# Kernel tuning notes

Measured on AMD Instinct MI355X. Metric: run time of the kernel, lower is better.

## Reference

```python
import jax, jax.numpy as jnp
import numpy as np

N = 4096          # nodes
IN_F = 256        # in_features (divisible by 4)
OUT_F = 64        # out_features per head
HEADS = 4
ALPHA = 0.2       # LeakyReLU negative slope
NEG_INF = -9e15   # same masking constant as the torch code


def make_quaternion_mul(kernel):
    """kernel: [IN_F//4, OUT_F] -> hamilton: [IN_F, OUT_F].
    Mirrors the torch make_quaternion_mul (split along dim=1 into r,i,j,k)."""
    r, i, j, k = jnp.split(kernel, 4, axis=1)
    r2 = jnp.concatenate([r, -i, -j, -k], axis=1)
    i2 = jnp.concatenate([i,  r, -k,  j], axis=1)
    j2 = jnp.concatenate([j,  k,  r, -i], axis=1)
    k2 = jnp.concatenate([k, -j,  i,  r], axis=1)
    return jnp.concatenate([r2, i2, j2, k2], axis=0)


def setup_inputs() -> dict:
    key = jax.random.key(0)
    k1, k2, k3, k4 = jax.random.split(key, 4)
    x = jax.random.normal(k1, (N, IN_F), dtype=jnp.float32)
    # Glorot-ish init for quaternion kernels: [H, IN_F//4, OUT_F]
    stdv = np.sqrt(6.0 / (IN_F // 4 + OUT_F)).astype(np.float32)
    W_heads = jax.random.uniform(k2, (HEADS, IN_F // 4, OUT_F), dtype=jnp.float32,
                                 minval=-stdv, maxval=stdv)
    a_heads = jax.random.normal(k3, (HEADS, 2 * OUT_F), dtype=jnp.float32) * 0.1
    adj = (jax.random.uniform(k4, (N, N)) < 0.005).astype(jnp.float32)
    adj = jnp.maximum(adj, jnp.eye(N, dtype=jnp.float32))
    return {"x": x, "adj": adj, "W_heads": W_heads, "a_heads": a_heads}


def reference(x, adj, W_heads, a_heads):
    mask = adj > 0  # [N, N]

    def head(Wk, ak):
        hamilton = make_quaternion_mul(Wk)                # [IN_F, OUT_F]
        h = x @ hamilton                                  # [N, OUT_F]
        # e[i,j] = leakyrelu(h_i . a[:F] + h_j . a[F:]) -- equivalent to the
        # repeat/concat construction without materializing [N*N, 2F].
        e_src = h @ ak[:OUT_F]                            # [N]
        e_dst = h @ ak[OUT_F:]                            # [N]
        e = jax.nn.leaky_relu(e_src[:, None] + e_dst[None, :], negative_slope=ALPHA)
        att = jax.nn.softmax(jnp.where(mask, e, NEG_INF), axis=1)  # [N, N]
        return att @ h                                    # [N, OUT_F]

    outs = jax.vmap(head)(W_heads, a_heads)               # [H, N, OUT_F]
    out = jnp.transpose(outs, (1, 0, 2)).reshape(N, HEADS * OUT_F)
    return jax.nn.elu(out)  # concat=True path
```

## Files before the change

### kernel.cpp

```cpp
#include <hip/hip_runtime.h>

#define N 4096
#define IN_F 256
#define OUT_F 64
#define HEADS 4
#define ALPHA 0.2f
#define SEG 64
#define LSTRIDE 320

typedef __attribute__((ext_vector_type(8))) short short8;
typedef __attribute__((ext_vector_type(4))) float f32x4;

__device__ __forceinline__ unsigned short f2bf(float f) {
    unsigned u = __builtin_bit_cast(unsigned, f);
    u += 0x7fffu + ((u >> 16) & 1u);
    return (unsigned short)(u >> 16);
}

__device__ __forceinline__ float bf2f(unsigned short u) {
    return __builtin_bit_cast(float, (unsigned)u << 16);
}

__global__ __launch_bounds__(256) void k_main(const float* __restrict__ x,
                                              const float* __restrict__ adj,
                                              const float* __restrict__ W,
                                              const float* __restrict__ a,
                                              unsigned short* __restrict__ hb,
                                              float* __restrict__ esp,
                                              float* __restrict__ edp,
                                              int* __restrict__ lists) {
    __shared__ int s_seg[4][SEG];
    __shared__ int s_cnt[4];
    __shared__ int s_all[4 * SEG];

    const int wave = threadIdx.x >> 6, lane = threadIdx.x & 63;
    const int i = blockIdx.x;

    if (wave == (i & 3)) {
        const int gw = i;
        const int rg = gw >> 4;
        const int hd = (gw >> 2) & 3;
        const int cq = gw & 3;
        const int m0 = rg * 16;
        const int r16 = lane & 15, g = lane >> 4;

        const int   comp_t[4][4] = {{0,1,2,3},{1,0,3,2},{2,3,0,1},{3,2,1,0}};
        const float sign_t[4][4] = {{1.f,-1.f,-1.f,-1.f},
                                    {1.f, 1.f,-1.f, 1.f},
                                    {1.f, 1.f, 1.f,-1.f},
                                    {1.f,-1.f, 1.f, 1.f}};

        const float* xrow = x + (size_t)(m0 + r16) * IN_F + g * 8;
        short8 af[8];
#pragma unroll
        for (int kk = 0; kk < 8; ++kk) {
            const float4 u0 = *reinterpret_cast<const float4*>(xrow + kk * 32);
            const float4 u1 = *reinterpret_cast<const float4*>(xrow + kk * 32 + 4);
            short8 t;
            t[0] = (short)f2bf(u0.x); t[1] = (short)f2bf(u0.y);
            t[2] = (short)f2bf(u0.z); t[3] = (short)f2bf(u0.w);
            t[4] = (short)f2bf(u1.x); t[5] = (short)f2bf(u1.y);
            t[6] = (short)f2bf(u1.z); t[7] = (short)f2bf(u1.w);
            af[kk] = t;
        }

        short8 bfr[8];
#pragma unroll
        for (int kk = 0; kk < 8; ++kk) {
            const int q = kk >> 1;
            const int kr0 = (kk & 1) * 32 + g * 8;
            const float s = sign_t[q][cq];
            const int c = comp_t[q][cq];
            const float* wp = W + (size_t)(hd * 64 + kr0) * 64 + c * 16 + r16;
            short8 t;
#pragma unroll
            for (int j = 0; j < 8; ++j) t[j] = (short)f2bf(s * wp[j * 64]);
            bfr[kk] = t;
        }

        f32x4 acc = (f32x4){0.f, 0.f, 0.f, 0.f};
#pragma unroll
        for (int kk = 0; kk < 8; ++kk)
            acc = __builtin_amdgcn_mfma_f32_16x16x32_bf16(af[kk], bfr[kk], acc, 0, 0, 0);

        const int f = cq * 16 + r16;
        const float as = a[hd * 128 + f];
        const float ad = a[hd * 128 + 64 + f];
        float p[4], q2[4];
#pragma unroll
        for (int j = 0; j < 4; ++j) {
            const float v = acc[j];
            hb[(size_t)(m0 + g * 4 + j) * (HEADS * OUT_F) + hd * 64 + f] = f2bf(v);
            p[j] = v * as;
            q2[j] = v * ad;
        }
#pragma unroll
        for (int off = 1; off < 16; off <<= 1) {
#pragma unroll
            for (int j = 0; j < 4; ++j) {
                p[j] += __shfl_xor(p[j], off);
                q2[j] += __shfl_xor(q2[j], off);
            }
        }
        if (r16 == 0) {
#pragma unroll
            for (int j = 0; j < 4; ++j) {
                const int row = m0 + g * 4 + j;
                esp[row * 16 + hd * 4 + cq] = p[j];
                edp[row * 16 + hd * 4 + cq] = q2[j];
            }
        }
    }

    const uint4* arow = reinterpret_cast<const uint4*>(adj + (size_t)i * N) + wave * 256;
    uint4 av[4];
#pragma unroll
    for (int c = 0; c < 4; ++c) av[c] = arow[c * 64 + lane];

    const unsigned long long lmask_lt = (lane == 63) ? ~0ull >> 1
                                                     : (1ull << lane) - 1ull;
    int base = 0;
#pragma unroll
    for (int c = 0; c < 4; ++c) {
#pragma unroll
        for (int s = 0; s < 4; ++s) {
            const unsigned v = (s == 0) ? av[c].x : (s == 1) ? av[c].y
                             : (s == 2) ? av[c].z : av[c].w;
            const bool hit = v != 0u;
            const unsigned long long mk = __ballot(hit);
            if (hit) {
                const int pos = base + __popcll(mk & lmask_lt);
                if (pos < SEG)
                    s_seg[wave][pos] = wave * 1024 + c * 256 + lane * 4 + s;
            }
            base += __popcll(mk);
        }
    }
    if (lane == 0) s_cnt[wave] = base < SEG ? base : SEG;
    __syncthreads();

    const int c0 = s_cnt[0], c1 = s_cnt[1], c2 = s_cnt[2], c3 = s_cnt[3];
    const int wbase = (wave > 0 ? c0 : 0) + (wave > 1 ? c1 : 0) + (wave > 2 ? c2 : 0);
    const int wcnt = s_cnt[wave];
    if (lane < wcnt) s_all[wbase + lane] = s_seg[wave][lane];
    __syncthreads();
    const int cnt = c0 + c1 + c2 + c3;

    if (threadIdx.x == 0) lists[(size_t)i * LSTRIDE] = cnt;
    for (int t = threadIdx.x; t < cnt; t += 256)
        lists[(size_t)i * LSTRIDE + 1 + t] = s_all[t];
}

__global__ __launch_bounds__(256) void k_out(const unsigned short* __restrict__ hb,
                                             const float* __restrict__ esp,
                                             const float* __restrict__ edp,
                                             const int* __restrict__ lists,
                                             float* __restrict__ out) {
    __shared__ int   s_all[4 * SEG];
    __shared__ float s_z[4][4 * SEG];

    const int wave = threadIdx.x >> 6;
    const int lane = threadIdx.x & 63;
    const int i = blockIdx.x;

    const int cnt = lists[(size_t)i * LSTRIDE];
    for (int t = threadIdx.x; t < cnt; t += 256)
        s_all[t] = lists[(size_t)i * LSTRIDE + 1 + t];
    __syncthreads();

    const int hd = wave;
    const float4 es4 = *reinterpret_cast<const float4*>(&esp[i * 16 + hd * 4]);
    const float es = (es4.x + es4.y) + (es4.z + es4.w);
    float mh = -3.0e38f;
    for (int e = lane; e < cnt; e += 64) {
        const int j = s_all[e];
        const float4 ed4 = *reinterpret_cast<const float4*>(&edp[j * 16 + hd * 4]);
        const float ed = (ed4.x + ed4.y) + (ed4.z + ed4.w);
        float z = es + ed;
        z = z > 0.f ? z : ALPHA * z;
        s_z[hd][e] = z;
        mh = fmaxf(mh, z);
    }
#pragma unroll
    for (int off = 32; off > 0; off >>= 1) mh = fmaxf(mh, __shfl_xor(mh, off));

    float lsum = 0.f, acc = 0.f;
    int e = 0;
    for (; e + 4 <= cnt; e += 4) {
        const int j0 = s_all[e], j1 = s_all[e + 1], j2 = s_all[e + 2], j3 = s_all[e + 3];
        const unsigned short u0 = hb[(size_t)j0 * 256 + threadIdx.x];
        const unsigned short u1 = hb[(size_t)j1 * 256 + threadIdx.x];
        const unsigned short u2 = hb[(size_t)j2 * 256 + threadIdx.x];
        const unsigned short u3 = hb[(size_t)j3 * 256 + threadIdx.x];
        const float w0 = __expf(s_z[hd][e]     - mh);
        const float w1 = __expf(s_z[hd][e + 1] - mh);
        const float w2 = __expf(s_z[hd][e + 2] - mh);
        const float w3 = __expf(s_z[hd][e + 3] - mh);
        lsum += w0 + w1 + w2 + w3;
        acc = fmaf(w0, bf2f(u0), acc);
        acc = fmaf(w1, bf2f(u1), acc);
        acc = fmaf(w2, bf2f(u2), acc);
        acc = fmaf(w3, bf2f(u3), acc);
    }
    for (; e < cnt; ++e) {
        const int j = s_all[e];
        const unsigned short u = hb[(size_t)j * 256 + threadIdx.x];
        const float w = __expf(s_z[hd][e] - mh);
        lsum += w;
        acc = fmaf(w, bf2f(u), acc);
    }

    const float v = acc / lsum;
    out[(size_t)i * 256 + threadIdx.x] = v > 0.f ? v : __expf(v) - 1.f;
}

extern "C" void kernel_launch(void* const* d_in, const int* in_sizes, int n_in,
                              void* d_out, int out_size, void* d_ws, size_t ws_size,
                              hipStream_t stream) {
    const float* x   = (const float*)d_in[0];
    const float* adj = (const float*)d_in[1];
    const float* W   = (const float*)d_in[2];
    const float* a   = (const float*)d_in[3];
    float* out = (float*)d_out;

    float* ws  = (float*)d_ws;
    float* esp = ws;
    float* edp = esp + N * 16;
    unsigned short* hb = (unsigned short*)(edp + N * 16);
    int* lists = (int*)(hb + (size_t)N * 256);

    k_main<<<N, 256, 0, stream>>>(x, adj, W, a, hb, esp, edp, lists);
    k_out<<<N, 256, 0, stream>>>(hb, esp, edp, lists, out);
}
```

Before: 38.07 us.

## Process four rows per block in both kernels and use all waves for GEMM

Both kernels now launch N/4 blocks, each looping over four adjacency rows, instead of one block per row. In k_main every wave of a block now does one GEMM tile, where before only one wave per block did. The aim is to cut block launch and scheduling overhead and idle waves. In exchange there are fewer blocks, so less parallelism and latency hiding across CUs, and each block runs its row loop serially with extra barriers.

```diff
diff --git a/kernel.cpp b/kernel.cpp
--- a/kernel.cpp
+++ b/kernel.cpp
@@ -7,6 +7,7 @@
 #define ALPHA 0.2f
 #define SEG 64
 #define LSTRIDE 320
+#define RPB 4
 
 typedef __attribute__((ext_vector_type(8))) short short8;
 typedef __attribute__((ext_vector_type(4))) float f32x4;
@@ -34,15 +35,15 @@
     __shared__ int s_all[4 * SEG];
 
     const int wave = threadIdx.x >> 6, lane = threadIdx.x & 63;
-    const int i = blockIdx.x;
-
-    if (wave == (i & 3)) {
-        const int gw = i;
+    const int g = blockIdx.x;
+
+    {
+        const int gw = g * 4 + wave;
         const int rg = gw >> 4;
         const int hd = (gw >> 2) & 3;
         const int cq = gw & 3;
         const int m0 = rg * 16;
-        const int r16 = lane & 15, g = lane >> 4;
+        const int r16 = lane & 15, g4 = lane >> 4;
 
         const int   comp_t[4][4] = {{0,1,2,3},{1,0,3,2},{2,3,0,1},{3,2,1,0}};
         const float sign_t[4][4] = {{1.f,-1.f,-1.f,-1.f},
@@ -50,7 +51,7 @@
                                     {1.f, 1.f, 1.f,-1.f},
                                     {1.f,-1.f, 1.f, 1.f}};
 
-        const float* xrow = x + (size_t)(m0 + r16) * IN_F + g * 8;
+        const float* xrow = x + (size_t)(m0 + r16) * IN_F + g4 * 8;
         short8 af[8];
 #pragma unroll
         for (int kk = 0; kk < 8; ++kk) {
@@ -68,7 +69,7 @@
 #pragma unroll
         for (int kk = 0; kk < 8; ++kk) {
             const int q = kk >> 1;
-            const int kr0 = (kk & 1) * 32 + g * 8;
+            const int kr0 = (kk & 1) * 32 + g4 * 8;
             const float s = sign_t[q][cq];
             const int c = comp_t[q][cq];
             const float* wp = W + (size_t)(hd * 64 + kr0) * 64 + c * 16 + r16;
@@ -90,7 +91,7 @@
 #pragma unroll
         for (int j = 0; j < 4; ++j) {
             const float v = acc[j];
-            hb[(size_t)(m0 + g * 4 + j) * (HEADS * OUT_F) + hd * 64 + f] = f2bf(v);
+            hb[(size_t)(m0 + g4 * 4 + j) * (HEADS * OUT_F) + hd * 64 + f] = f2bf(v);
             p[j] = v * as;
             q2[j] = v * ad;
         }
@@ -105,50 +106,55 @@
         if (r16 == 0) {
 #pragma unroll
             for (int j = 0; j < 4; ++j) {
-                const int row = m0 + g * 4 + j;
+                const int row = m0 + g4 * 4 + j;
                 esp[row * 16 + hd * 4 + cq] = p[j];
                 edp[row * 16 + hd * 4 + cq] = q2[j];
             }
         }
     }
 
-    const uint4* arow = reinterpret_cast<const uint4*>(adj + (size_t)i * N) + wave * 256;
-    uint4 av[4];
-#pragma unroll
-    for (int c = 0; c < 4; ++c) av[c] = arow[c * 64 + lane];
-
     const unsigned long long lmask_lt = (lane == 63) ? ~0ull >> 1
                                                      : (1ull << lane) - 1ull;
-    int base = 0;
-#pragma unroll
-    for (int c = 0; c < 4; ++c) {
-#pragma unroll
-        for (int s = 0; s < 4; ++s) {
-            const unsigned v = (s == 0) ? av[c].x : (s == 1) ? av[c].y
-                             : (s == 2) ? av[c].z : av[c].w;
-            const bool hit = v != 0u;
-            const unsigned long long mk = __ballot(hit);
-            if (hit) {
-                const int pos = base + __popcll(mk & lmask_lt);
-                if (pos < SEG)
-                    s_seg[wave][pos] = wave * 1024 + c * 256 + lane * 4 + s;
+    for (int r = 0; r < RPB; ++r) {
+        const int i = g * RPB + r;
+        if (r) __syncthreads();
+
+        const uint4* arow = reinterpret_cast<const uint4*>(adj + (size_t)i * N) + wave * 256;
+        uint4 av[4];
+#pragma unroll
+        for (int c = 0; c < 4; ++c) av[c] = arow[c * 64 + lane];
+
+        int base = 0;
+#pragma unroll
+        for (int c = 0; c < 4; ++c) {
+#pragma unroll
+            for (int s = 0; s < 4; ++s) {
+                const unsigned v = (s == 0) ? av[c].x : (s == 1) ? av[c].y
+                                 : (s == 2) ? av[c].z : av[c].w;
+                const bool hit = v != 0u;
+                const unsigned long long mk = __ballot(hit);
+                if (hit) {
+                    const int pos = base + __popcll(mk & lmask_lt);
+                    if (pos < SEG)
+                        s_seg[wave][pos] = wave * 1024 + c * 256 + lane * 4 + s;
+                }
+                base += __popcll(mk);
             }
-            base += __popcll(mk);
-        }
+        }
+        if (lane == 0) s_cnt[wave] = base < SEG ? base : SEG;
+        __syncthreads();
+
+        const int c0 = s_cnt[0], c1 = s_cnt[1], c2 = s_cnt[2], c3 = s_cnt[3];
+        const int wbase = (wave > 0 ? c0 : 0) + (wave > 1 ? c1 : 0) + (wave > 2 ? c2 : 0);
+        const int wcnt = s_cnt[wave];
+        if (lane < wcnt) s_all[wbase + lane] = s_seg[wave][lane];
+        __syncthreads();
+        const int cnt = c0 + c1 + c2 + c3;
+
+        if (threadIdx.x == 0) lists[(size_t)i * LSTRIDE] = cnt;
+        for (int t = threadIdx.x; t < cnt; t += 256)
+            lists[(size_t)i * LSTRIDE + 1 + t] = s_all[t];
     }
-    if (lane == 0) s_cnt[wave] = base < SEG ? base : SEG;
-    __syncthreads();
-
-    const int c0 = s_cnt[0], c1 = s_cnt[1], c2 = s_cnt[2], c3 = s_cnt[3];
-    const int wbase = (wave > 0 ? c0 : 0) + (wave > 1 ? c1 : 0) + (wave > 2 ? c2 : 0);
-    const int wcnt = s_cnt[wave];
-    if (lane < wcnt) s_all[wbase + lane] = s_seg[wave][lane];
-    __syncthreads();
-    const int cnt = c0 + c1 + c2 + c3;
-
-    if (threadIdx.x == 0) lists[(size_t)i * LSTRIDE] = cnt;
-    for (int t = threadIdx.x; t < cnt; t += 256)
-        lists[(size_t)i * LSTRIDE + 1 + t] = s_all[t];
 }
 
 __global__ __launch_bounds__(256) void k_out(const unsigned short* __restrict__ hb,
@@ -161,57 +167,62 @@
 
     const int wave = threadIdx.x >> 6;
     const int lane = threadIdx.x & 63;
-    const int i = blockIdx.x;
-
-    const int cnt = lists[(size_t)i * LSTRIDE];
-    for (int t = threadIdx.x; t < cnt; t += 256)
-        s_all[t] = lists[(size_t)i * LSTRIDE + 1 + t];
-    __syncthreads();
-
-    const int hd = wave;
-    const float4 es4 = *reinterpret_cast<const float4*>(&esp[i * 16 + hd * 4]);
-    const float es = (es4.x + es4.y) + (es4.z + es4.w);
-    float mh = -3.0e38f;
-    for (int e = lane; e < cnt; e += 64) {
-        const int j = s_all[e];
-        const float4 ed4 = *reinterpret_cast<const float4*>(&edp[j * 16 + hd * 4]);
-        const float ed = (ed4.x + ed4.y) + (ed4.z + ed4.w);
-        float z = es + ed;
-        z = z > 0.f ? z : ALPHA * z;
-        s_z[hd][e] = z;
-        mh = fmaxf(mh, z);
+    const int g = blockIdx.x;
+
+    for (int r = 0; r < RPB; ++r) {
+        const int i = g * RPB + r;
+        if (r) __syncthreads();
+
+        const int cnt = lists[(size_t)i * LSTRIDE];
+        for (int t = threadIdx.x; t < cnt; t += 256)
+            s_all[t] = lists[(size_t)i * LSTRIDE + 1 + t];
+        __syncthreads();
+
+        const int hd = wave;
+        const float4 es4 = *reinterpret_cast<const float4*>(&esp[i * 16 + hd * 4]);
+        const float es = (es4.x + es4.y) + (es4.z + es4.w);
+        float mh = -3.0e38f;
+        for (int e = lane; e < cnt; e += 64) {
+            const int j = s_all[e];
+            const float4 ed4 = *reinterpret_cast<const float4*>(&edp[j * 16 + hd * 4]);
+            const float ed = (ed4.x + ed4.y) + (ed4.z + ed4.w);
+            float z = es + ed;
+            z = z > 0.f ? z : ALPHA * z;
+            s_z[hd][e] = z;
+            mh = fmaxf(mh, z);
+        }
+#pragma unroll
+        for (int off = 32; off > 0; off >>= 1) mh = fmaxf(mh, __shfl_xor(mh, off));
+
+        float lsum = 0.f, acc = 0.f;
+        int e = 0;
+        for (; e + 4 <= cnt; e += 4) {
+            const int j0 = s_all[e], j1 = s_all[e + 1], j2 = s_all[e + 2], j3 = s_all[e + 3];
+            const unsigned short u0 = hb[(size_t)j0 * 256 + threadIdx.x];
+            const unsigned short u1 = hb[(size_t)j1 * 256 + threadIdx.x];
+            const unsigned short u2 = hb[(size_t)j2 * 256 + threadIdx.x];
+            const unsigned short u3 = hb[(size_t)j3 * 256 + threadIdx.x];
+            const float w0 = __expf(s_z[hd][e]     - mh);
+            const float w1 = __expf(s_z[hd][e + 1] - mh);
+            const float w2 = __expf(s_z[hd][e + 2] - mh);
+            const float w3 = __expf(s_z[hd][e + 3] - mh);
+            lsum += w0 + w1 + w2 + w3;
+            acc = fmaf(w0, bf2f(u0), acc);
+            acc = fmaf(w1, bf2f(u1), acc);
+            acc = fmaf(w2, bf2f(u2), acc);
+            acc = fmaf(w3, bf2f(u3), acc);
+        }
+        for (; e < cnt; ++e) {
+            const int j = s_all[e];
+            const unsigned short u = hb[(size_t)j * 256 + threadIdx.x];
+            const float w = __expf(s_z[hd][e] - mh);
+            lsum += w;
+            acc = fmaf(w, bf2f(u), acc);
+        }
+
+        const float v = acc / lsum;
+        out[(size_t)i * 256 + threadIdx.x] = v > 0.f ? v : __expf(v) - 1.f;
     }
-#pragma unroll
-    for (int off = 32; off > 0; off >>= 1) mh = fmaxf(mh, __shfl_xor(mh, off));
-
-    float lsum = 0.f, acc = 0.f;
-    int e = 0;
-    for (; e + 4 <= cnt; e += 4) {
-        const int j0 = s_all[e], j1 = s_all[e + 1], j2 = s_all[e + 2], j3 = s_all[e + 3];
-        const unsigned short u0 = hb[(size_t)j0 * 256 + threadIdx.x];
-        const unsigned short u1 = hb[(size_t)j1 * 256 + threadIdx.x];
-        const unsigned short u2 = hb[(size_t)j2 * 256 + threadIdx.x];
-        const unsigned short u3 = hb[(size_t)j3 * 256 + threadIdx.x];
-        const float w0 = __expf(s_z[hd][e]     - mh);
-        const float w1 = __expf(s_z[hd][e + 1] - mh);
-        const float w2 = __expf(s_z[hd][e + 2] - mh);
-        const float w3 = __expf(s_z[hd][e + 3] - mh);
-        lsum += w0 + w1 + w2 + w3;
-        acc = fmaf(w0, bf2f(u0), acc);
-        acc = fmaf(w1, bf2f(u1), acc);
-        acc = fmaf(w2, bf2f(u2), acc);
-        acc = fmaf(w3, bf2f(u3), acc);
-    }
-    for (; e < cnt; ++e) {
-        const int j = s_all[e];
-        const unsigned short u = hb[(size_t)j * 256 + threadIdx.x];
-        const float w = __expf(s_z[hd][e] - mh);
-        lsum += w;
-        acc = fmaf(w, bf2f(u), acc);
-    }
-
-    const float v = acc / lsum;
-    out[(size_t)i * 256 + threadIdx.x] = v > 0.f ? v : __expf(v) - 1.f;
 }
 
 extern "C" void kernel_launch(void* const* d_in, const int* in_sizes, int n_in,
@@ -229,6 +240,6 @@
     unsigned short* hb = (unsigned short*)(edp + N * 16);
     int* lists = (int*)(hb + (size_t)N * 256);
 
-    k_main<<<N, 256, 0, stream>>>(x, adj, W, a, hb, esp, edp, lists);
-    k_out<<<N, 256, 0, stream>>>(hb, esp, edp, lists, out);
-}
+    k_main<<<N / RPB, 256, 0, stream>>>(x, adj, W, a, hb, esp, edp, lists);
+    k_out<<<N / RPB, 256, 0, stream>>>(hb, esp, edp, lists, out);
+}
```

Measured after the change: 41.96 us. +10.2%, slower.
